# Optimization experiments

Measured on AMD Instinct MI355X. Metric: run time of the kernel, lower is better.

Reference implementation:

```python
import jax, jax.numpy as jnp
import numpy as np

D_MODEL = 1024
N_HEADS = 16
HEAD_DIM = D_MODEL // N_HEADS
SOFTMAX_SCALE = 1.0 / np.sqrt(HEAD_DIM).astype(np.float32)


def setup_inputs() -> dict:
    key = jax.random.key(0)
    k1, k2, k3, k4, k5 = jax.random.split(key, 5)
    B, S = 2, 2048
    bound_qkv = 1.0 / np.sqrt(D_MODEL)
    x = jax.random.normal(k1, (B, S, D_MODEL), dtype=jnp.float32)
    # torch nn.Linear stores weight as [out_features, in_features]
    Wqkv_w = jax.random.uniform(k2, (3 * D_MODEL, D_MODEL), jnp.float32, -bound_qkv, bound_qkv)
    Wqkv_b = jax.random.uniform(k3, (3 * D_MODEL,), jnp.float32, -bound_qkv, bound_qkv)
    Wout_w = jax.random.uniform(k4, (D_MODEL, D_MODEL), jnp.float32, -bound_qkv, bound_qkv)
    Wout_b = jax.random.uniform(k5, (D_MODEL,), jnp.float32, -bound_qkv, bound_qkv)
    return {"x": x, "Wqkv_w": Wqkv_w, "Wqkv_b": Wqkv_b, "Wout_w": Wout_w, "Wout_b": Wout_b}


def reference(x, Wqkv_w, Wqkv_b, Wout_w, Wout_b):
    B, S, D = x.shape
    # fused QKV projection
    qkv = jnp.einsum('bsd,ed->bse', x, Wqkv_w) + Wqkv_b  # [B, S, 3D]
    q, k, v = jnp.split(qkv, 3, axis=2)
    # b s (h d) -> b h s d
    q = q.reshape(B, S, N_HEADS, HEAD_DIM).transpose(0, 2, 1, 3)
    k = k.reshape(B, S, N_HEADS, HEAD_DIM).transpose(0, 2, 1, 3)
    v = v.reshape(B, S, N_HEADS, HEAD_DIM).transpose(0, 2, 1, 3)
    attn = jnp.einsum('bhsd,bhtd->bhst', q, k) * SOFTMAX_SCALE
    attn = jax.nn.softmax(attn, axis=-1)
    ctx = jnp.einsum('bhst,bhtd->bhsd', attn, v)
    ctx = ctx.transpose(0, 2, 1, 3).reshape(B, S, D)
    out = jnp.einsum('bsd,ed->bse', ctx, Wout_w) + Wout_b
    return out
```

## Files before the change

### kernel.cpp

```cpp
#include <hip/hip_runtime.h>
#include <hip/hip_bf16.h>

typedef __attribute__((ext_vector_type(8))) __bf16 bfrag;
typedef __attribute__((ext_vector_type(4))) float f32x4;
typedef __attribute__((ext_vector_type(16))) float f32x16;
typedef __attribute__((ext_vector_type(8))) unsigned short u16x8;
typedef __attribute__((ext_vector_type(4))) unsigned short u16x4;
typedef __attribute__((ext_vector_type(4))) unsigned int u32x4;

#define SEQ 2048
#define NH 16
#define HD 64
#define DMODEL 1024
#define MTOT 4096
#define QSCALE 0.18033688011112042f

static __device__ __forceinline__ unsigned short f2bf(float f) {
  unsigned int u = __builtin_bit_cast(unsigned int, f);
  u += 0x7FFFu + ((u >> 16) & 1u);
  return (unsigned short)(u >> 16);
}

static __device__ __forceinline__ unsigned cvt_pk_bf16(float lo, float hi) {
  unsigned r;
  asm("v_cvt_pk_bf16_f32 %0, %1, %2" : "=v"(r) : "v"(lo), "v"(hi));
  return r;
}

static __device__ __forceinline__ float rsum16(const f32x16 v) {
  float a0 = v[0] + v[1], a1 = v[2] + v[3], a2 = v[4] + v[5], a3 = v[6] + v[7];
  float a4 = v[8] + v[9], a5 = v[10] + v[11], a6 = v[12] + v[13], a7 = v[14] + v[15];
  float b0 = a0 + a1, b1 = a2 + a3, b2 = a4 + a5, b3 = a6 + a7;
  return (b0 + b1) + (b2 + b3);
}

#define XG 524288
#define WQG 393216
#define WOG 131072
__global__ __launch_bounds__(256) void cvt_all_kernel(const float* __restrict__ x,
                                                      const float* __restrict__ wq,
                                                      const float* __restrict__ wo,
                                                      unsigned short* __restrict__ out) {
  int i = blockIdx.x * 256 + threadIdx.x;
  if (i >= XG + WQG + WOG) return;
  const float4* p;
  if (i < XG) p = reinterpret_cast<const float4*>(x) + (size_t)i * 2;
  else if (i < XG + WQG) p = reinterpret_cast<const float4*>(wq) + (size_t)(i - XG) * 2;
  else p = reinterpret_cast<const float4*>(wo) + (size_t)(i - XG - WQG) * 2;
  float4 a = p[0], b = p[1];
  u16x8 o;
  o[0] = f2bf(a.x); o[1] = f2bf(a.y); o[2] = f2bf(a.z); o[3] = f2bf(a.w);
  o[4] = f2bf(b.x); o[5] = f2bf(b.y); o[6] = f2bf(b.z); o[7] = f2bf(b.w);
  *(reinterpret_cast<u16x8*>(out) + i) = o;
}

#define GLDS(gp, lp)                                                       \
  __builtin_amdgcn_global_load_lds(                                        \
      (const __attribute__((address_space(1))) void*)(gp),                 \
      (__attribute__((address_space(3))) void*)(lp), 16, 0, 0)

template <int EPI>
__global__ __launch_bounds__(256) void gemm_bt_kernel(
    const unsigned short* __restrict__ A, const unsigned short* __restrict__ B,
    const float* __restrict__ bias, unsigned short* __restrict__ q_out,
    unsigned short* __restrict__ k_out, unsigned short* __restrict__ v_out,
    float* __restrict__ f_out, int M, int N, int K) {
  __shared__ __align__(16) unsigned short As[3][4096];
  __shared__ __align__(16) unsigned short Bs[3][4096];
  const int t = threadIdx.x;
  const int l = t & 63, w = t >> 6;
  const int m0 = blockIdx.y * 128, n0 = blockIdx.x * 128;
  const int wrow = (w >> 1) * 64, wcol = (w & 1) * 64;
  const int lrow = l & 15, lk = (l >> 4) * 8;
  const int srow = t >> 2;
  const int scol = ((t & 3) ^ (srow & 3)) * 8;
  f32x4 acc[4][4] = {};

#define GSTAGE(buf, K0)                                                     \
  do {                                                                      \
    GLDS(A + (size_t)(m0 + srow) * K + (K0) + scol, &As[buf][0] + t * 8);   \
    GLDS(A + (size_t)(m0 + srow + 64) * K + (K0) + scol,                    \
         &As[buf][0] + 2048 + t * 8);                                       \
    GLDS(B + (size_t)(n0 + srow) * K + (K0) + scol, &Bs[buf][0] + t * 8);   \
    GLDS(B + (size_t)(n0 + srow + 64) * K + (K0) + scol,                    \
         &Bs[buf][0] + 2048 + t * 8);                                       \
  } while (0)

  const int nsteps = K >> 5;
  GSTAGE(0, 0);
  GSTAGE(1, 32);
#pragma unroll 1
  for (int ks = 0; ks < nsteps; ++ks) {
    if (ks < nsteps - 1)
      asm volatile("s_waitcnt vmcnt(4)" ::: "memory");
    else
      asm volatile("s_waitcnt vmcnt(0)" ::: "memory");
    __builtin_amdgcn_s_barrier();
    __builtin_amdgcn_sched_barrier(0);
    if (ks + 2 < nsteps) GSTAGE((ks + 2) % 3, (ks + 2) * 32);
    const unsigned short* Ac = &As[ks % 3][0];
    const unsigned short* Bc = &Bs[ks % 3][0];
    bfrag af[4], bf[4];
#pragma unroll
    for (int mt = 0; mt < 4; ++mt) {
      int row = wrow + mt * 16 + lrow;
      af[mt] = *(const bfrag*)&Ac[row * 32 + (lk ^ ((row & 3) << 3))];
    }
#pragma unroll
    for (int nt = 0; nt < 4; ++nt) {
      int row = wcol + nt * 16 + lrow;
      bf[nt] = *(const bfrag*)&Bc[row * 32 + (lk ^ ((row & 3) << 3))];
    }
#pragma unroll
    for (int mt = 0; mt < 4; ++mt)
#pragma unroll
      for (int nt = 0; nt < 4; ++nt)
        acc[mt][nt] =
            __builtin_amdgcn_mfma_f32_16x16x32_bf16(af[mt], bf[nt], acc[mt][nt], 0, 0, 0);
  }
#undef GSTAGE
#pragma unroll
  for (int nt = 0; nt < 4; ++nt) {
    int gn = n0 + wcol + nt * 16 + lrow;
    float bv = bias[gn];
    if constexpr (EPI == 0) {
      int sel = gn >> 10;
      int e = gn & 1023;
      int h = e >> 6, d = e & 63;
#pragma unroll
      for (int mt = 0; mt < 4; ++mt) {
#pragma unroll
        for (int r = 0; r < 4; ++r) {
          int gm = m0 + wrow + mt * 16 + (l >> 4) * 4 + r;
          int b = gm >> 11, s = gm & 2047;
          float fv = acc[mt][nt][r] + bv;
          if (sel == 0)
            q_out[((size_t)(b * NH + h) * SEQ + s) * HD + d] = f2bf(fv * QSCALE);
          else if (sel == 1)
            k_out[((size_t)(b * NH + h) * SEQ + s) * HD + d] = f2bf(fv);
          else
            v_out[((size_t)(b * NH + h) * HD + d) * SEQ + s] = f2bf(fv);
        }
      }
    } else {
#pragma unroll
      for (int mt = 0; mt < 4; ++mt) {
#pragma unroll
        for (int r = 0; r < 4; ++r) {
          int gm = m0 + wrow + mt * 16 + (l >> 4) * 4 + r;
          f_out[(size_t)gm * N + gn] = acc[mt][nt][r] + bv;
        }
      }
    }
  }
}

__global__ __launch_bounds__(256, 2)
void attn_kernel(const unsigned short* __restrict__ Q,
                 const unsigned short* __restrict__ Km,
                 const unsigned short* __restrict__ Vt,
                 unsigned short* __restrict__ Ctx) {
  __shared__ __align__(16) unsigned short Ks[2][128 * 64];
  __shared__ __align__(16) unsigned short Vs[2][64 * 128];
  const int t = threadIdx.x;
  const int l = t & 63, w = t >> 6;
  const int q31 = l & 31, h = l >> 5;
  const int lid = blockIdx.y * gridDim.x + blockIdx.x;
  const int bh = (lid & 7) * 4 + ((lid >> 3) >> 4);
  const int q0 = ((lid >> 3) & 15) * 128 + w * 32;
  const unsigned short* qb = Q + (size_t)bh * SEQ * HD;
  const unsigned short* kb = Km + (size_t)bh * SEQ * HD;
  const unsigned short* vb = Vt + (size_t)bh * HD * SEQ;

  bfrag qf[4];
#pragma unroll
  for (int c = 0; c < 4; ++c)
    qf[c] = *(const bfrag*)&qb[(size_t)(q0 + q31) * HD + c * 16 + h * 8];

  f32x16 acc0 = {}, acc1 = {};
  float llocal = 0.f;

  const int skr = t >> 3;
  const int sks = ((t & 7) ^ (skr & 7)) * 8;
  const int svr = t >> 4;
  const int svs = ((t & 15) ^ svr) * 8;

#define STAGE(buf, T)                                                          \
  do {                                                                         \
    const int kv0_ = (T) * 128;                                                \
    _Pragma("unroll") for (int j = 0; j < 4; ++j)                              \
        GLDS(kb + (size_t)(kv0_ + 32 * j + skr) * HD + sks,                    \
             &Ks[buf][0] + j * 2048 + t * 8);                                  \
    _Pragma("unroll") for (int j = 0; j < 4; ++j)                              \
        GLDS(vb + (size_t)(16 * j + svr) * SEQ + kv0_ + svs,                   \
             &Vs[buf][0] + j * 2048 + t * 8);                                  \
  } while (0)

  STAGE(0, 0);
  __syncthreads();

  const int sw7 = q31 & 7, sw15 = q31 & 15;
  const int st0 = w & 3;

#define LOADK(kfv, stx)                                                        \
  _Pragma("unroll") for (int c = 0; c < 4; ++c)                                \
      kfv[c] = *(const bfrag*)&Kc[((stx) * 32 + q31) * 64 +                    \
                                  (((2 * c + h) ^ sw7) * 8)]

#define QK4(dst, kfv)                                                          \
  do {                                                                         \
    dst = (f32x16){};                                                          \
    __builtin_amdgcn_s_setprio(1);                                             \
    _Pragma("unroll") for (int c = 0; c < 4; ++c)                              \
        dst = __builtin_amdgcn_mfma_f32_32x32x16_bf16(kfv[c], qf[c], dst, 0, 0, 0); \
    __builtin_amdgcn_s_setprio(0);                                             \
  } while (0)

#define SOFTPV(stx, SV)                                                        \
  do {                                                                         \
    _Pragma("unroll") for (int r = 0; r < 16; ++r)                             \
        SV[r] = __builtin_amdgcn_exp2f(SV[r]);                                 \
    llocal += rsum16(SV);                                                      \
    _Pragma("unroll") for (int u = 0; u < 2; ++u) {                            \
      const int win = (stx) * 2 + u;                                           \
      const int bse = u * 8;                                                   \
      unsigned pk0 = cvt_pk_bf16(SV[bse + 0], SV[bse + 1]);                    \
      unsigned pk1 = cvt_pk_bf16(SV[bse + 2], SV[bse + 3]);                    \
      unsigned pk2 = cvt_pk_bf16(SV[bse + 4], SV[bse + 5]);                    \
      unsigned pk3 = cvt_pk_bf16(SV[bse + 6], SV[bse + 7]);                    \
      auto w02 = __builtin_amdgcn_permlane32_swap(pk0, pk2, false, false);     \
      auto w13 = __builtin_amdgcn_permlane32_swap(pk1, pk3, false, false);     \
      u32x4 bw = {(unsigned)w02[0], (unsigned)w13[0], (unsigned)w02[1],        \
                  (unsigned)w13[1]};                                           \
      bfrag pb = __builtin_bit_cast(bfrag, bw);                                \
      const int vchunk = ((win * 2 + h) ^ sw15) * 8;                           \
      bfrag vf0 = *(const bfrag*)&Vc[q31 * 128 + vchunk];                      \
      bfrag vf1 = *(const bfrag*)&Vc[(32 + q31) * 128 + vchunk];               \
      __builtin_amdgcn_s_setprio(1);                                           \
      acc0 = __builtin_amdgcn_mfma_f32_32x32x16_bf16(vf0, pb, acc0, 0, 0, 0);  \
      acc1 = __builtin_amdgcn_mfma_f32_32x32x16_bf16(vf1, pb, acc1, 0, 0, 0);  \
      __builtin_amdgcn_s_setprio(0);                                           \
    }                                                                          \
  } while (0)

#pragma unroll 1
  for (int t2 = 0; t2 < 16; ++t2) {
    const unsigned short* Kc = &Ks[t2 & 1][0];
    const unsigned short* Vc = &Vs[t2 & 1][0];
    bfrag kfa[4], kfb[4];
    f32x16 scur, snxt;
    LOADK(kfa, st0);
    QK4(scur, kfa);
    if (t2 < 15) STAGE((t2 + 1) & 1, t2 + 1);
#pragma unroll
    for (int j = 0; j < 4; ++j) {
      if (j < 3) {
        const int stn = (st0 + j + 1) & 3;
        LOADK(kfb, stn);
        QK4(snxt, kfb);
      }
      const int stc = (st0 + j) & 3;
      SOFTPV(stc, scur);
      scur = snxt;
    }
    __syncthreads();
  }
#undef STAGE
#undef LOADK
#undef QK4
#undef SOFTPV

  const int b = bh >> 4, head = bh & 15;
  float lsum = llocal + __shfl_xor(llocal, 32);
  const float inv = __builtin_amdgcn_rcpf(lsum);
  unsigned short* cp = Ctx + ((size_t)(b * SEQ + (q0 + q31)) * NH + head) * HD;
#pragma unroll
  for (int dt = 0; dt < 2; ++dt) {
    const f32x16 av = dt ? acc1 : acc0;
#pragma unroll
    for (int rq = 0; rq < 4; ++rq) {
      u16x4 o;
#pragma unroll
      for (int rr = 0; rr < 4; ++rr) o[rr] = f2bf(av[rq * 4 + rr] * inv);
      *(u16x4*)&cp[dt * 32 + rq * 8 + h * 4] = o;
    }
  }
}

extern "C" void kernel_launch(void* const* d_in, const int* in_sizes, int n_in,
                              void* d_out, int out_size, void* d_ws, size_t ws_size,
                              hipStream_t stream) {
  const float* x = (const float*)d_in[0];
  const float* wqkv = (const float*)d_in[1];
  const float* bqkv = (const float*)d_in[2];
  const float* wout = (const float*)d_in[3];
  const float* bout = (const float*)d_in[4];
  float* out = (float*)d_out;

  unsigned short* xb = (unsigned short*)d_ws;
  unsigned short* wqkvb = xb + (size_t)MTOT * DMODEL;
  unsigned short* woutb = wqkvb + (size_t)3 * DMODEL * DMODEL;
  unsigned short* qb = woutb + (size_t)DMODEL * DMODEL;
  unsigned short* kb = qb + (size_t)32 * SEQ * HD;
  unsigned short* vtb = kb + (size_t)32 * SEQ * HD;
  unsigned short* ctxb = vtb + (size_t)32 * SEQ * HD;

  cvt_all_kernel<<<(XG + WQG + WOG + 255) / 256, 256, 0, stream>>>(x, wqkv, wout, xb);
  gemm_bt_kernel<0><<<dim3(3 * DMODEL / 128, MTOT / 128), 256, 0, stream>>>(
      xb, wqkvb, bqkv, qb, kb, vtb, nullptr, MTOT, 3 * DMODEL, DMODEL);
  attn_kernel<<<dim3(SEQ / 128, 32), 256, 0, stream>>>(qb, kb, vtb, ctxb);
  gemm_bt_kernel<1><<<dim3(DMODEL / 128, MTOT / 128), 256, 0, stream>>>(
      ctxb, woutb, bout, nullptr, nullptr, nullptr, out, MTOT, DMODEL, DMODEL);
}
```

Baseline: 120.2 us.

## Use 256x256 tiled 512-thread GEMM for the QKV projection

Replaces the 128x128 QKV projection GEMM with a dedicated kernel that uses 256x256 output tiles, 8 waves, BK=64 double buffering, XOR-swizzled LDS and a remapped block order for L2 locality. The larger tile raises arithmetic intensity and cuts global/LDS traffic per FLOP. It leaves only 192 blocks, which on a 256-CU part leaves CUs idle, and it uses 128KB LDS plus large register pressure. The output GEMM is split into its own non-templated kernel.

```diff
diff --git a/kernel.cpp b/kernel.cpp
--- a/kernel.cpp
+++ b/kernel.cpp
@@ -59,12 +59,137 @@
       (const __attribute__((address_space(1))) void*)(gp),                 \
       (__attribute__((address_space(3))) void*)(lp), 16, 0, 0)
 
-template <int EPI>
-__global__ __launch_bounds__(256) void gemm_bt_kernel(
+__global__ __launch_bounds__(512, 2)
+void gemm256_qkv_kernel(const unsigned short* __restrict__ A,
+                        const unsigned short* __restrict__ B,
+                        const float* __restrict__ bias,
+                        unsigned short* __restrict__ q_out,
+                        unsigned short* __restrict__ k_out,
+                        unsigned short* __restrict__ v_out) {
+  __shared__ __align__(16) unsigned short As[2][256 * 64];
+  __shared__ __align__(16) unsigned short Bs[2][256 * 64];
+  const int K = 1024;
+  const int t = threadIdx.x;
+  const int l = t & 63, wid = t >> 6;
+  const int wm = wid >> 2, wn = wid & 3;
+  const int lrow = l & 15, hi = l >> 4;
+  const int lid0 = blockIdx.y * 12 + blockIdx.x;
+  const int lid = (lid0 & 7) * 24 + (lid0 >> 3);
+  const int n0 = (lid % 12) * 256, m0 = (lid / 12) * 256;
+  const int sr = t >> 3;
+  const int sc = ((t & 7) ^ (sr & 7)) * 8;
+
+#define STG(buf, kt)                                                        \
+  do {                                                                      \
+    const int kk = (kt) * 64;                                               \
+    _Pragma("unroll") for (int j = 0; j < 4; ++j)                           \
+        GLDS(A + (size_t)(m0 + j * 64 + sr) * K + kk + sc,                  \
+             &As[buf][0] + j * 4096 + t * 8);                               \
+    _Pragma("unroll") for (int j = 0; j < 4; ++j)                           \
+        GLDS(B + (size_t)(n0 + j * 64 + sr) * K + kk + sc,                  \
+             &Bs[buf][0] + j * 4096 + t * 8);                               \
+  } while (0)
+
+  f32x4 acc[8][4] = {};
+  const int rsw = lrow & 7;
+  const int ch0 = ((0 * 4 + hi) ^ rsw) * 8;
+  const int ch1 = ((1 * 4 + hi) ^ rsw) * 8;
+  const int arow0 = wm * 128 + lrow;
+  const int brow0 = wn * 64 + lrow;
+
+  STG(0, 0);
+  __syncthreads();
+
+#pragma unroll 1
+  for (int kt = 0; kt < 16; ++kt) {
+    if (kt < 15) STG((kt + 1) & 1, kt + 1);
+    const unsigned short* Ac = &As[kt & 1][0];
+    const unsigned short* Bc = &Bs[kt & 1][0];
+    bfrag a0[4][2], a1[4][2], b0[2][2], b1[2][2];
+#pragma unroll
+    for (int mt = 0; mt < 4; ++mt) {
+      a0[mt][0] = *(const bfrag*)&Ac[(arow0 + mt * 16) * 64 + ch0];
+      a0[mt][1] = *(const bfrag*)&Ac[(arow0 + mt * 16) * 64 + ch1];
+    }
+#pragma unroll
+    for (int nt = 0; nt < 2; ++nt) {
+      b0[nt][0] = *(const bfrag*)&Bc[(brow0 + nt * 16) * 64 + ch0];
+      b0[nt][1] = *(const bfrag*)&Bc[(brow0 + nt * 16) * 64 + ch1];
+    }
+#pragma unroll
+    for (int mt = 0; mt < 4; ++mt)
+#pragma unroll
+      for (int nt = 0; nt < 2; ++nt)
+#pragma unroll
+        for (int ks = 0; ks < 2; ++ks)
+          acc[mt][nt] = __builtin_amdgcn_mfma_f32_16x16x32_bf16(a0[mt][ks], b0[nt][ks],
+                                                                acc[mt][nt], 0, 0, 0);
+#pragma unroll
+    for (int nt = 0; nt < 2; ++nt) {
+      b1[nt][0] = *(const bfrag*)&Bc[(brow0 + (nt + 2) * 16) * 64 + ch0];
+      b1[nt][1] = *(const bfrag*)&Bc[(brow0 + (nt + 2) * 16) * 64 + ch1];
+    }
+#pragma unroll
+    for (int mt = 0; mt < 4; ++mt)
+#pragma unroll
+      for (int nt = 0; nt < 2; ++nt)
+#pragma unroll
+        for (int ks = 0; ks < 2; ++ks)
+          acc[mt][nt + 2] = __builtin_amdgcn_mfma_f32_16x16x32_bf16(
+              a0[mt][ks], b1[nt][ks], acc[mt][nt + 2], 0, 0, 0);
+#pragma unroll
+    for (int mt = 0; mt < 4; ++mt) {
+      a1[mt][0] = *(const bfrag*)&Ac[(arow0 + (mt + 4) * 16) * 64 + ch0];
+      a1[mt][1] = *(const bfrag*)&Ac[(arow0 + (mt + 4) * 16) * 64 + ch1];
+    }
+#pragma unroll
+    for (int mt = 0; mt < 4; ++mt)
+#pragma unroll
+      for (int nt = 0; nt < 2; ++nt)
+#pragma unroll
+        for (int ks = 0; ks < 2; ++ks)
+          acc[mt + 4][nt + 2] = __builtin_amdgcn_mfma_f32_16x16x32_bf16(
+              a1[mt][ks], b1[nt][ks], acc[mt + 4][nt + 2], 0, 0, 0);
+#pragma unroll
+    for (int mt = 0; mt < 4; ++mt)
+#pragma unroll
+      for (int nt = 0; nt < 2; ++nt)
+#pragma unroll
+        for (int ks = 0; ks < 2; ++ks)
+          acc[mt + 4][nt] = __builtin_amdgcn_mfma_f32_16x16x32_bf16(
+              a1[mt][ks], b0[nt][ks], acc[mt + 4][nt], 0, 0, 0);
+    __syncthreads();
+  }
+#undef STG
+
+#pragma unroll
+  for (int nt = 0; nt < 4; ++nt) {
+    const int gn = n0 + wn * 64 + nt * 16 + lrow;
+    const float bv = bias[gn];
+    const int sel = gn >> 10;
+    const int e = gn & 1023;
+    const int hh = e >> 6, d = e & 63;
+#pragma unroll
+    for (int mt = 0; mt < 8; ++mt) {
+#pragma unroll
+      for (int r = 0; r < 4; ++r) {
+        const int gm = m0 + wm * 128 + mt * 16 + hi * 4 + r;
+        const int b = gm >> 11, s = gm & 2047;
+        const float fv = acc[mt][nt][r] + bv;
+        if (sel == 0)
+          q_out[((size_t)(b * NH + hh) * SEQ + s) * HD + d] = f2bf(fv * QSCALE);
+        else if (sel == 1)
+          k_out[((size_t)(b * NH + hh) * SEQ + s) * HD + d] = f2bf(fv);
+        else
+          v_out[((size_t)(b * NH + hh) * HD + d) * SEQ + s] = f2bf(fv);
+      }
+    }
+  }
+}
+
+__global__ __launch_bounds__(256) void gemm_out_kernel(
     const unsigned short* __restrict__ A, const unsigned short* __restrict__ B,
-    const float* __restrict__ bias, unsigned short* __restrict__ q_out,
-    unsigned short* __restrict__ k_out, unsigned short* __restrict__ v_out,
-    float* __restrict__ f_out, int M, int N, int K) {
+    const float* __restrict__ bias, float* __restrict__ f_out, int M, int N, int K) {
   __shared__ __align__(16) unsigned short As[3][4096];
   __shared__ __align__(16) unsigned short Bs[3][4096];
   const int t = threadIdx.x;
@@ -123,33 +248,12 @@
   for (int nt = 0; nt < 4; ++nt) {
     int gn = n0 + wcol + nt * 16 + lrow;
     float bv = bias[gn];
-    if constexpr (EPI == 0) {
-      int sel = gn >> 10;
-      int e = gn & 1023;
-      int h = e >> 6, d = e & 63;
-#pragma unroll
-      for (int mt = 0; mt < 4; ++mt) {
-#pragma unroll
-        for (int r = 0; r < 4; ++r) {
-          int gm = m0 + wrow + mt * 16 + (l >> 4) * 4 + r;
-          int b = gm >> 11, s = gm & 2047;
-          float fv = acc[mt][nt][r] + bv;
-          if (sel == 0)
-            q_out[((size_t)(b * NH + h) * SEQ + s) * HD + d] = f2bf(fv * QSCALE);
-          else if (sel == 1)
-            k_out[((size_t)(b * NH + h) * SEQ + s) * HD + d] = f2bf(fv);
-          else
-            v_out[((size_t)(b * NH + h) * HD + d) * SEQ + s] = f2bf(fv);
-        }
-      }
-    } else {
-#pragma unroll
-      for (int mt = 0; mt < 4; ++mt) {
-#pragma unroll
-        for (int r = 0; r < 4; ++r) {
-          int gm = m0 + wrow + mt * 16 + (l >> 4) * 4 + r;
-          f_out[(size_t)gm * N + gn] = acc[mt][nt][r] + bv;
-        }
+#pragma unroll
+    for (int mt = 0; mt < 4; ++mt) {
+#pragma unroll
+      for (int r = 0; r < 4; ++r) {
+        int gm = m0 + wrow + mt * 16 + (l >> 4) * 4 + r;
+        f_out[(size_t)gm * N + gn] = acc[mt][nt][r] + bv;
       }
     }
   }
@@ -306,9 +410,8 @@
   unsigned short* ctxb = vtb + (size_t)32 * SEQ * HD;
 
   cvt_all_kernel<<<(XG + WQG + WOG + 255) / 256, 256, 0, stream>>>(x, wqkv, wout, xb);
-  gemm_bt_kernel<0><<<dim3(3 * DMODEL / 128, MTOT / 128), 256, 0, stream>>>(
-      xb, wqkvb, bqkv, qb, kb, vtb, nullptr, MTOT, 3 * DMODEL, DMODEL);
+  gemm256_qkv_kernel<<<dim3(12, 16), 512, 0, stream>>>(xb, wqkvb, bqkv, qb, kb, vtb);
   attn_kernel<<<dim3(SEQ / 128, 32), 256, 0, stream>>>(qb, kb, vtb, ctxb);
-  gemm_bt_kernel<1><<<dim3(DMODEL / 128, MTOT / 128), 256, 0, stream>>>(
-      ctxb, woutb, bout, nullptr, nullptr, nullptr, out, MTOT, DMODEL, DMODEL);
-}
+  gemm_out_kernel<<<dim3(DMODEL / 128, MTOT / 128), 256, 0, stream>>>(
+      ctxb, woutb, bout, out, MTOT, DMODEL, DMODEL);
+}
```

Result: slower. 135.3 us (+12.6%).
